# Optimization experiments

Hardware: AMD Instinct MI355X
Metric: run time of the kernel (lower is better)

## Reference

```python
import jax, jax.numpy as jnp
import numpy as np

N_EMBED = 384
N_HEAD = 6
HEAD_DIM = N_EMBED // N_HEAD


def setup_inputs() -> dict:
    key = jax.random.key(0)
    k1, k2, k3 = jax.random.split(key, 3)
    B, T = 128, 256
    x = jax.random.normal(k1, (B, T, N_EMBED), dtype=jnp.float32)
    # nn.Linear(N_EMBED, 3*N_EMBED, bias=False): weight [3*N_EMBED, N_EMBED],
    # applied as x @ W.T -> store transposed [N_EMBED, 3*N_EMBED]
    W_qkv = jax.random.normal(k2, (N_EMBED, 3 * N_EMBED), dtype=jnp.float32) * (N_EMBED ** -0.5)
    W_proj = jax.random.normal(k3, (N_EMBED, N_EMBED), dtype=jnp.float32) * (N_EMBED ** -0.5)
    return {"x": x, "W_qkv": W_qkv, "W_proj": W_proj}


def reference(x, W_qkv, W_proj):
    B, T, C = x.shape
    qkv = jnp.einsum('btc,cd->btd', x, W_qkv)  # [B,T,3C]
    q, k, v = jnp.split(qkv, 3, axis=-1)
    # [B, H, T, Dh]
    q = q.reshape(B, T, N_HEAD, HEAD_DIM).transpose(0, 2, 1, 3)
    k = k.reshape(B, T, N_HEAD, HEAD_DIM).transpose(0, 2, 1, 3)
    v = v.reshape(B, T, N_HEAD, HEAD_DIM).transpose(0, 2, 1, 3)
    scale = HEAD_DIM ** -0.5
    wei = jnp.einsum('bhqd,bhkd->bhqk', q, k) * scale  # [B,H,T,T]
    causal = jnp.tril(jnp.ones((T, T), dtype=bool))
    wei = jnp.where(causal[None, None, :, :], wei, -jnp.inf)
    wei = jax.nn.softmax(wei, axis=-1)
    # dropout layers are identity in eval mode
    out = jnp.einsum('bhqk,bhkd->bhqd', wei, v)  # [B,H,T,Dh]
    out = out.transpose(0, 2, 1, 3).reshape(B, T, C)
    out = jnp.einsum('btc,cd->btd', out, W_proj)
    return out
```

## Files before the change

### kernel.cpp

```cpp
#include <hip/hip_runtime.h>
#include <hip/hip_bf16.h>

typedef __attribute__((ext_vector_type(8))) short short8;
typedef __attribute__((ext_vector_type(4))) float f32x4;
typedef __attribute__((ext_vector_type(4))) unsigned short ush4;

typedef const __attribute__((address_space(1))) void* gas_p;
typedef __attribute__((address_space(3))) void* las_p;
#define GLOAD_LDS16(g, l) __builtin_amdgcn_global_load_lds((gas_p)(const void*)(g), (las_p)(void*)(l), 16, 0, 0)

__device__ __forceinline__ unsigned short f2bf(float f) {
    union { float f; unsigned int u; } v; v.f = f;
    unsigned int r = v.u + 0x7FFFu + ((v.u >> 16) & 1u);
    return (unsigned short)(r >> 16);
}
__device__ __forceinline__ unsigned pk2(float a, float b) {
    return (unsigned)f2bf(a) | ((unsigned)f2bf(b) << 16);
}

__global__ __launch_bounds__(256) void cast_wt_kernel(
    const float* __restrict__ W, unsigned short* __restrict__ Wt, int K, int N)
{
    int idx = blockIdx.x * 256 + threadIdx.x;
    if (idx >= N * K) return;
    int n = idx / K, k = idx - n * K;
    Wt[idx] = f2bf(W[(size_t)k * N + n]);
}

__global__ __launch_bounds__(256, 2) void gemm_qkv_kernel(
    const float* __restrict__ x,
    const unsigned short* __restrict__ Bt,
    unsigned short* __restrict__ qkb,
    unsigned short* __restrict__ vtb)
{
    const int K = 384;
    __shared__ __align__(16) unsigned short Sh[2 * 128 * 64];
    unsigned short* As = Sh;
    unsigned short* Bs = Sh + 128 * 64;
    const int tid = threadIdx.x;
    const int lane = tid & 63, wv = tid >> 6;
    const int c = lane & 15, g = lane >> 4;
    const int wm = (wv >> 1) * 64, wn = (wv & 1) * 64;

    const int id = blockIdx.x, xcd = id & 7, kk = id >> 3;
    const long m0 = (long)(xcd * 32 + kk / 9) * 128;
    const long n0 = (long)(kk % 9) * 128;

    f32x4 acc[4][4] = {};
    const int xr = (c & 7) << 4;

    for (int kt = 0; kt < K; kt += 64) {
        #pragma unroll
        for (int i = 0; i < 4; ++i) {
            int ch = i * 256 + tid;
            int row = ch >> 3, cc = ch & 7;
            GLOAD_LDS16(&Bt[(n0 + row) * (size_t)K + kt + (cc ^ (row & 7)) * 8],
                        &Bs[(i * 256 + wv * 64) * 8]);
        }
        #pragma unroll
        for (int i = 0; i < 4; ++i) {
            int ch = i * 256 + tid;
            int row = ch >> 3, cc = ch & 7;
            const float* ga = &x[(m0 + row) * (size_t)K + kt + (cc ^ (row & 7)) * 8];
            float4 a = *(const float4*)ga;
            float4 b = *(const float4*)(ga + 4);
            uint4 w;
            w.x = pk2(a.x, a.y); w.y = pk2(a.z, a.w);
            w.z = pk2(b.x, b.y); w.w = pk2(b.z, b.w);
            *(uint4*)&As[ch * 8] = w;
        }
        __syncthreads();
        #pragma unroll
        for (int ks = 0; ks < 2; ++ks) {
            short8 af[4], bf_[4];
            #pragma unroll
            for (int i = 0; i < 4; ++i)
                af[i] = *(const short8*)((char*)As +
                    (((wm + i * 16 + c) * 128 + (ks * 32 + g * 8) * 2) ^ xr));
            #pragma unroll
            for (int i = 0; i < 4; ++i)
                bf_[i] = *(const short8*)((char*)Bs +
                    (((wn + i * 16 + c) * 128 + (ks * 32 + g * 8) * 2) ^ xr));
            #pragma unroll
            for (int mi = 0; mi < 4; ++mi)
                #pragma unroll
                for (int ni = 0; ni < 4; ++ni)
                    acc[mi][ni] = __builtin_amdgcn_mfma_f32_16x16x32_bf16(
                        af[mi], bf_[ni], acc[mi][ni], 0, 0, 0);
        }
        __syncthreads();
    }

    if (n0 < 768) {
        #pragma unroll
        for (int mi = 0; mi < 4; ++mi)
            #pragma unroll
            for (int ni = 0; ni < 4; ++ni)
                #pragma unroll
                for (int r = 0; r < 4; ++r) {
                    long m = m0 + wm + mi * 16 + g * 4 + r;
                    long n = n0 + wn + ni * 16 + c;
                    qkb[m * 768 + n] = f2bf(acc[mi][ni][r]);
                }
    } else {
        char* wbase = (char*)Sh + wv * 8192;
        #pragma unroll
        for (int ni = 0; ni < 4; ++ni)
            #pragma unroll
            for (int mi = 0; mi < 4; ++mi)
                #pragma unroll
                for (int r = 0; r < 4; ++r) {
                    int d = ni * 16 + c, t = mi * 16 + g * 4 + r;
                    int byte = (d * 128 + t * 2) ^ ((d & 7) << 4);
                    *(unsigned short*)(wbase + byte) = f2bf(acc[mi][ni][r]);
                }
        __asm__ __volatile__("" ::: "memory");
        int h = (int)((n0 + wn - 768) >> 6);
        long b = (m0 + wm) >> 8;
        int t0 = (int)((m0 + wm) & 255);
        long bh = b * 6 + h;
        #pragma unroll
        for (int it = 0; it < 8; ++it) {
            int d = it * 8 + (lane >> 3), ck = lane & 7;
            short8 v = *(const short8*)(wbase + ((d * 128 + ck * 16) ^ ((d & 7) << 4)));
            *(short8*)&vtb[(bh * 64 + d) * 256 + t0 + ck * 8] = v;
        }
    }
}

__global__ __launch_bounds__(256, 2) void gemm_proj_kernel(
    const unsigned short* __restrict__ A, const unsigned short* __restrict__ Bt,
    float* __restrict__ C, int M, int N, int K)
{
    __shared__ __align__(16) unsigned short As[128 * 64];
    __shared__ __align__(16) unsigned short Bs[128 * 64];
    const int tid = threadIdx.x;
    const int lane = tid & 63, wv = tid >> 6;
    const int c = lane & 15, g = lane >> 4;
    const int wm = (wv >> 1) * 64, wn = (wv & 1) * 64;

    const int mpx = (M >> 7) >> 3;
    const int id = blockIdx.x, xcd = id & 7, kk = id >> 3;
    const long m0 = (long)(xcd * mpx + (kk % mpx)) * 128;
    const long n0 = (long)(kk / mpx) * 128;

    f32x4 acc[4][4] = {};
    const int xr = (c & 7) << 4;

    for (int kt = 0; kt < K; kt += 64) {
        #pragma unroll
        for (int i = 0; i < 4; ++i) {
            int ch = i * 256 + wv * 64 + lane;
            int row = ch >> 3, cc = ch & 7;
            int sc = (cc ^ (row & 7)) * 8;
            GLOAD_LDS16(&A[(m0 + row) * (size_t)K + kt + sc],
                        &As[(i * 256 + wv * 64) * 8]);
            GLOAD_LDS16(&Bt[(n0 + row) * (size_t)K + kt + sc],
                        &Bs[(i * 256 + wv * 64) * 8]);
        }
        __syncthreads();
        #pragma unroll
        for (int ks = 0; ks < 2; ++ks) {
            short8 af[4], bf_[4];
            #pragma unroll
            for (int i = 0; i < 4; ++i)
                af[i] = *(const short8*)((char*)As +
                    (((wm + i * 16 + c) * 128 + (ks * 32 + g * 8) * 2) ^ xr));
            #pragma unroll
            for (int i = 0; i < 4; ++i)
                bf_[i] = *(const short8*)((char*)Bs +
                    (((wn + i * 16 + c) * 128 + (ks * 32 + g * 8) * 2) ^ xr));
            #pragma unroll
            for (int mi = 0; mi < 4; ++mi)
                #pragma unroll
                for (int ni = 0; ni < 4; ++ni)
                    acc[mi][ni] = __builtin_amdgcn_mfma_f32_16x16x32_bf16(
                        af[mi], bf_[ni], acc[mi][ni], 0, 0, 0);
        }
        __syncthreads();
    }

    #pragma unroll
    for (int mi = 0; mi < 4; ++mi)
        #pragma unroll
        for (int ni = 0; ni < 4; ++ni)
            #pragma unroll
            for (int r = 0; r < 4; ++r) {
                long m = m0 + wm + mi * 16 + g * 4 + r;
                long n = n0 + wn + ni * 16 + c;
                C[m * N + n] = acc[mi][ni][r];
            }
}

__global__ __launch_bounds__(256, 3) void attn_kernel(
    const unsigned short* __restrict__ qk,
    const unsigned short* __restrict__ vt,
    unsigned short* __restrict__ outp)
{
    const int bh = blockIdx.x;
    const int b = bh / 6, h = bh - b * 6;
    const int tid = threadIdx.x;
    const int lane = tid & 63, wv = tid >> 6;
    const int c = lane & 15, g = lane >> 4;

    __shared__ unsigned short Ks[256 * 64];
    __shared__ unsigned short Pl[4][16 * 64];

    #pragma unroll
    for (int it = 0; it < 8; ++it) {
        int ch = it * 256 + tid;
        int row = ch >> 3, col = (ch & 7) * 8;
        int db = (row * 128 + col * 2) ^ ((row & 7) << 4);
        *(short8*)((char*)Ks + db) =
            *(const short8*)&qk[(size_t)(b * 256 + row) * 768 + 384 + h * 64 + col];
    }
    __syncthreads();

    char* plw = (char*)Pl[wv];

    for (int t = 0; t < 2; ++t) {
        const int p = t ? 7 - wv : wv;
        const int jlast = p >> 1;
        const int modd = (p & 1) * 32;
        const int qt0 = p * 32;

        short8 aq[2][2];
        #pragma unroll
        for (int mi = 0; mi < 2; ++mi)
            #pragma unroll
            for (int ks = 0; ks < 2; ++ks)
                aq[mi][ks] = *(const short8*)&qk[
                    (size_t)(b * 256 + qt0 + mi * 16 + c) * 768 + h * 64 + ks * 32 + g * 8];

        f32x4 o[2][4] = {};
        float mrun[2] = {-1e30f, -1e30f}, lrun[2] = {0.f, 0.f};

        for (int j = 0; j <= jlast; ++j) {
            short8 bv[4][2];
            #pragma unroll
            for (int nd = 0; nd < 4; ++nd)
                #pragma unroll
                for (int ks = 0; ks < 2; ++ks)
                    bv[nd][ks] = *(const short8*)&vt[
                        ((size_t)bh * 64 + nd * 16 + c) * 256 + j * 64 + ks * 32 + g * 8];

            short8 bk[4][2];
            #pragma unroll
            for (int ni = 0; ni < 4; ++ni)
                #pragma unroll
                for (int ks = 0; ks < 2; ++ks) {
                    int key = j * 64 + ni * 16 + c;
                    bk[ni][ks] = *(const short8*)((char*)Ks +
                        ((key * 128 + (ks * 32 + g * 8) * 2) ^ ((key & 7) << 4)));
                }

            #pragma unroll
            for (int mi = 0; mi < 2; ++mi) {
                float pv[4][4];
                #pragma unroll
                for (int ni = 0; ni < 4; ++ni) {
                    f32x4 z = {0.f, 0.f, 0.f, 0.f};
                    z = __builtin_amdgcn_mfma_f32_16x16x32_bf16(bk[ni][0], aq[mi][0], z, 0, 0, 0);
                    z = __builtin_amdgcn_mfma_f32_16x16x32_bf16(bk[ni][1], aq[mi][1], z, 0, 0, 0);
                    #pragma unroll
                    for (int r = 0; r < 4; ++r) {
                        float v = z[r] * 0.125f;
                        if (j == jlast) {
                            int kloc = ni * 16 + g * 4 + r;
                            int qloc = mi * 16 + c + modd;
                            if (kloc > qloc) v = -1e30f;
                        }
                        pv[ni][r] = v;
                    }
                }
                float m01 = fmaxf(fmaxf(pv[0][0], pv[0][1]), fmaxf(pv[0][2], pv[0][3]));
                float m11 = fmaxf(fmaxf(pv[1][0], pv[1][1]), fmaxf(pv[1][2], pv[1][3]));
                float m21 = fmaxf(fmaxf(pv[2][0], pv[2][1]), fmaxf(pv[2][2], pv[2][3]));
                float m31 = fmaxf(fmaxf(pv[3][0], pv[3][1]), fmaxf(pv[3][2], pv[3][3]));
                float m1 = fmaxf(fmaxf(m01, m11), fmaxf(m21, m31));
                m1 = fmaxf(m1, __shfl_xor(m1, 16));
                m1 = fmaxf(m1, __shfl_xor(m1, 32));
                float mold = mrun[mi];
                float mnew = fmaxf(mold, m1);
                float fac = __expf(mold - mnew);
                float ssum = 0.f;
                #pragma unroll
                for (int ni = 0; ni < 4; ++ni)
                    #pragma unroll
                    for (int r = 0; r < 4; ++r) {
                        float pp = __expf(pv[ni][r] - mnew);
                        pv[ni][r] = pp;
                        ssum += pp;
                    }
                ssum += __shfl_xor(ssum, 16);
                ssum += __shfl_xor(ssum, 32);
                lrun[mi] = lrun[mi] * fac + ssum;
                mrun[mi] = mnew;
                #pragma unroll
                for (int nd = 0; nd < 4; ++nd)
                    #pragma unroll
                    for (int r = 0; r < 4; ++r) o[mi][nd][r] *= fac;

                __asm__ __volatile__("" ::: "memory");
                #pragma unroll
                for (int ni = 0; ni < 4; ++ni) {
                    uint2 w;
                    w.x = pk2(pv[ni][0], pv[ni][1]);
                    w.y = pk2(pv[ni][2], pv[ni][3]);
                    *(uint2*)(plw + ((c * 128 + ni * 32 + g * 8) ^ ((c & 7) << 4))) = w;
                }
                __asm__ __volatile__("" ::: "memory");

                short8 ap[2];
                #pragma unroll
                for (int ks = 0; ks < 2; ++ks)
                    ap[ks] = *(const short8*)(plw +
                        ((c * 128 + ks * 64 + g * 16) ^ ((c & 7) << 4)));

                #pragma unroll
                for (int nd = 0; nd < 4; ++nd) {
                    o[mi][nd] = __builtin_amdgcn_mfma_f32_16x16x32_bf16(bv[nd][0], ap[0], o[mi][nd], 0, 0, 0);
                    o[mi][nd] = __builtin_amdgcn_mfma_f32_16x16x32_bf16(bv[nd][1], ap[1], o[mi][nd], 0, 0, 0);
                }
                __asm__ __volatile__("" ::: "memory");
            }
        }

        #pragma unroll
        for (int mi = 0; mi < 2; ++mi) {
            float inv = 1.0f / lrun[mi];
            #pragma unroll
            for (int nd = 0; nd < 4; ++nd) {
                ush4 w;
                #pragma unroll
                for (int r = 0; r < 4; ++r) w[r] = f2bf(o[mi][nd][r] * inv);
                *(ush4*)&outp[((size_t)b * 256 + qt0 + mi * 16 + c) * 384 + h * 64 + nd * 16 + g * 4] = w;
            }
        }
    }
}

extern "C" void kernel_launch(void* const* d_in, const int* in_sizes, int n_in,
                              void* d_out, int out_size, void* d_ws, size_t ws_size,
                              hipStream_t stream) {
    const float* x     = (const float*)d_in[0];
    const float* Wqkv  = (const float*)d_in[1];
    const float* Wproj = (const float*)d_in[2];

    char* ws = (char*)d_ws;
    unsigned short* wqkvt  = (unsigned short*)(ws);
    unsigned short* wprojt = (unsigned short*)(ws + 884736);
    unsigned short* qkb    = (unsigned short*)(ws + 1179648);
    unsigned short* vtb    = (unsigned short*)(ws + 51511296);
    unsigned short* attnb  = (unsigned short*)(ws + 76677120);

    cast_wt_kernel<<<1728, 256, 0, stream>>>(Wqkv, wqkvt, 384, 1152);
    cast_wt_kernel<<<576, 256, 0, stream>>>(Wproj, wprojt, 384, 384);

    gemm_qkv_kernel<<<2304, 256, 0, stream>>>(x, wqkvt, qkb, vtb);
    attn_kernel<<<768, 256, 0, stream>>>(qkb, vtb, attnb);
    gemm_proj_kernel<<<768, 256, 0, stream>>>(attnb, wprojt, (float*)d_out, 32768, 384, 384);
}
```

Before: 125.1 us.

## Software-pipeline QKV GEMM: double-buffer B in LDS and prefetch A into registers

Restructures the QKV GEMM K-loop so the next tile's B is issued as async global-to-LDS loads into a second buffer, and the next A tile's fp32 values are loaded into registers, both while the current tile's MFMAs run. A is converted to bf16 and written to LDS after the compute barrier. This aims to hide global load latency behind the matrix math. In exchange it uses more LDS (three tiles instead of two), more registers for the prefetched A values, and an extra barrier per iteration, which may reduce occupancy.

```diff
diff --git a/kernel.cpp b/kernel.cpp
--- a/kernel.cpp
+++ b/kernel.cpp
@@ -34,9 +34,9 @@
     unsigned short* __restrict__ vtb)
 {
     const int K = 384;
-    __shared__ __align__(16) unsigned short Sh[2 * 128 * 64];
+    const int NT = 6;
+    __shared__ __align__(16) unsigned short Sh[3 * 128 * 64];
     unsigned short* As = Sh;
-    unsigned short* Bs = Sh + 128 * 64;
     const int tid = threadIdx.x;
     const int lane = tid & 63, wv = tid >> 6;
     const int c = lane & 15, g = lane >> 4;
@@ -49,27 +49,56 @@
     f32x4 acc[4][4] = {};
     const int xr = (c & 7) << 4;
 
-    for (int kt = 0; kt < K; kt += 64) {
-        #pragma unroll
-        for (int i = 0; i < 4; ++i) {
-            int ch = i * 256 + tid;
-            int row = ch >> 3, cc = ch & 7;
-            GLOAD_LDS16(&Bt[(n0 + row) * (size_t)K + kt + (cc ^ (row & 7)) * 8],
-                        &Bs[(i * 256 + wv * 64) * 8]);
-        }
-        #pragma unroll
-        for (int i = 0; i < 4; ++i) {
-            int ch = i * 256 + tid;
-            int row = ch >> 3, cc = ch & 7;
-            const float* ga = &x[(m0 + row) * (size_t)K + kt + (cc ^ (row & 7)) * 8];
-            float4 a = *(const float4*)ga;
-            float4 b = *(const float4*)(ga + 4);
-            uint4 w;
-            w.x = pk2(a.x, a.y); w.y = pk2(a.z, a.w);
-            w.z = pk2(b.x, b.y); w.w = pk2(b.z, b.w);
-            *(uint4*)&As[ch * 8] = w;
-        }
-        __syncthreads();
+    int chrow[4], chcc[4];
+    #pragma unroll
+    for (int i = 0; i < 4; ++i) {
+        int ch = i * 256 + tid;
+        chrow[i] = ch >> 3;
+        chcc[i] = ((ch & 7) ^ (chrow[i] & 7)) * 8;
+    }
+
+#define LOAD_A_REGS(kt)                                                        \
+    {                                                                          \
+        _Pragma("unroll")                                                      \
+        for (int i = 0; i < 4; ++i) {                                          \
+            const float* ga = &x[(m0 + chrow[i]) * (size_t)K + (kt) + chcc[i]];\
+            ar0[i] = *(const float4*)ga;                                       \
+            ar1[i] = *(const float4*)(ga + 4);                                 \
+        }                                                                      \
+    }
+#define WRITE_A_LDS()                                                          \
+    {                                                                          \
+        _Pragma("unroll")                                                      \
+        for (int i = 0; i < 4; ++i) {                                          \
+            uint4 w;                                                           \
+            w.x = pk2(ar0[i].x, ar0[i].y); w.y = pk2(ar0[i].z, ar0[i].w);      \
+            w.z = pk2(ar1[i].x, ar1[i].y); w.w = pk2(ar1[i].z, ar1[i].w);      \
+            *(uint4*)&As[(i * 256 + tid) * 8] = w;                             \
+        }                                                                      \
+    }
+#define STAGE_B(bufofs, kt)                                                    \
+    {                                                                          \
+        _Pragma("unroll")                                                      \
+        for (int i = 0; i < 4; ++i)                                            \
+            GLOAD_LDS16(&Bt[(n0 + chrow[i]) * (size_t)K + (kt) + chcc[i]],     \
+                        &Sh[(bufofs) + (i * 256 + wv * 64) * 8]);              \
+    }
+
+    float4 ar0[4], ar1[4];
+
+    LOAD_A_REGS(0);
+    STAGE_B(8192, 0);
+    WRITE_A_LDS();
+    __syncthreads();
+
+    for (int t = 0; t < NT; ++t) {
+        const int bofs = 8192 + (t & 1) * 8192;
+        const int nofs = 8192 + ((t + 1) & 1) * 8192;
+        if (t + 1 < NT) {
+            STAGE_B(nofs, (t + 1) * 64);
+            LOAD_A_REGS((t + 1) * 64);
+        }
+        const unsigned short* Bcur = Sh + bofs;
         #pragma unroll
         for (int ks = 0; ks < 2; ++ks) {
             short8 af[4], bf_[4];
@@ -79,7 +108,7 @@
                     (((wm + i * 16 + c) * 128 + (ks * 32 + g * 8) * 2) ^ xr));
             #pragma unroll
             for (int i = 0; i < 4; ++i)
-                bf_[i] = *(const short8*)((char*)Bs +
+                bf_[i] = *(const short8*)((char*)Bcur +
                     (((wn + i * 16 + c) * 128 + (ks * 32 + g * 8) * 2) ^ xr));
             #pragma unroll
             for (int mi = 0; mi < 4; ++mi)
@@ -89,7 +118,14 @@
                         af[mi], bf_[ni], acc[mi][ni], 0, 0, 0);
         }
         __syncthreads();
-    }
+        if (t + 1 < NT) {
+            WRITE_A_LDS();
+            __syncthreads();
+        }
+    }
+#undef LOAD_A_REGS
+#undef WRITE_A_LDS
+#undef STAGE_B
 
     if (n0 < 768) {
         #pragma unroll
```

Result: slower. 129.4 us (+3.5%).
